# Kernel tuning notes

Measured on AMD Instinct MI355X. Metric: run time of the kernel, lower is better.

The kernel has to match this reference:

```python
import jax, jax.numpy as jnp
import numpy as np

LOSS_WEIGHT = 1.0  # init kwarg


def _cdist2(a, b):
    # Euclidean (p=2) pairwise distances via Gram trick: avoids [n,m,d] tensor.
    d2 = (jnp.sum(a * a, axis=1)[:, None]
          + jnp.sum(b * b, axis=1)[None, :]
          - 2.0 * (a @ b.T))
    return jnp.sqrt(jnp.maximum(d2, 0.0))


def _clamp_comb(f, g):
    # Composition of clamp maps x -> clip(x, lo, hi); g is applied after f.
    lf, hf = f
    lg, hg = g
    return jnp.clip(lf, lg, hg), jnp.clip(hf, lg, hg)


def _frechet(pred, target):
    c = _cdist2(pred, target)                      # [n, m]
    # First DP row: running max of c[0, :].
    row0 = jax.lax.associative_scan(jnp.maximum, c[0])

    def row_update(prev, c_row):
        # ca[i,j] = max(min(ca[i-1,j], ca[i,j-1], ca[i-1,j-1]), c[i,j])
        # For fixed i this is d[j] = clip(d[j-1], lo=c[i,j], hi=max(b[j], c[i,j]))
        # with b[j] = min(prev[j], prev[j-1]); clamp composition is associative,
        # so the whole row is a parallel associative scan (wavefront-free form).
        d0 = jnp.maximum(prev[0], c_row[0])        # ca[i,0]
        lo = c_row[1:]
        hi = jnp.maximum(jnp.minimum(prev[1:], prev[:-1]), lo)
        lo_all = jnp.concatenate([d0[None], lo])   # element 0 is the constant map d0
        hi_all = jnp.concatenate([d0[None], hi])
        lo_s, _ = jax.lax.associative_scan(_clamp_comb, (lo_all, hi_all))
        return lo_s, None

    last_row, _ = jax.lax.scan(row_update, row0, c[1:])
    return last_row[-1]


def setup_inputs() -> dict:
    key = jax.random.key(0)
    k1, k2 = jax.random.split(key)
    pred = jax.random.uniform(k1, (4096, 128), dtype=jnp.float32)
    target = jax.random.uniform(k2, (4096, 128), dtype=jnp.float32)
    return {"pred": pred, "target": target}


def reference(pred, target):
    return LOSS_WEIGHT * _frechet(pred, target)
```

## Files before the change

kernel.cpp:

```cpp
#include <hip/hip_runtime.h>

typedef unsigned short u16;
typedef unsigned int u32;
typedef __bf16 bf16x8 __attribute__((ext_vector_type(8)));
typedef float f32x4 __attribute__((ext_vector_type(4)));

#define N 4096
#define KD 128
#define NSTRIP 32
#define W 128
#define ROWB 256
#define CH 32
#define STB 16
#define NBLK 132
#define HUGEV 3.0e38f
#define TS 128
#define PADK 136

__device__ __forceinline__ u16 f2bf(float v) {
  u32 u = __float_as_uint(v);
  u += 0x7fffu + ((u >> 16) & 1u);
  return (u16)(u >> 16);
}
__device__ __forceinline__ float bf2f(u16 b) { return __uint_as_float(((u32)b) << 16); }
__device__ __forceinline__ float bfround(float v) { return bf2f(f2bf(v)); }

__device__ __forceinline__ float dpp_shr1(float oldv, float src) {
  return __int_as_float(__builtin_amdgcn_update_dpp(
      __float_as_int(oldv), __float_as_int(src), 0x138, 0xF, 0xF, false));
}

__device__ __forceinline__ void gload_lds16(const void* g, void* l) {
  __builtin_amdgcn_global_load_lds((const __attribute__((address_space(1))) u32*)g,
                                   (__attribute__((address_space(3))) u32*)l, 16, 0, 0);
}

__global__ __launch_bounds__(256) void norms_kernel(const float* __restrict__ pred,
                                                    const float* __restrict__ tgt,
                                                    float* __restrict__ na, float* __restrict__ nb,
                                                    float* __restrict__ edgeG) {
  const int t = blockIdx.x * 256 + threadIdx.x;
  if (t < NSTRIP * N) edgeG[t] = -1.0f;
  int gw = blockIdx.x * 4 + (threadIdx.x >> 6);
  int lane = threadIdx.x & 63;
  const float* base = (gw < N) ? (pred + (size_t)gw * KD) : (tgt + (size_t)(gw - N) * KD);
  float2 v = ((const float2*)base)[lane];
  float x = bfround(v.x), y = bfround(v.y);
  float s = x * x + y * y;
  #pragma unroll
  for (int off = 32; off > 0; off >>= 1) s += __shfl_xor(s, off);
  if (lane == 0) { if (gw < N) na[gw] = s; else nb[gw - N] = s; }
}

__global__ __launch_bounds__(256) void gemm_kernel(const float* __restrict__ A, const float* __restrict__ B,
                                                   const float* __restrict__ na, const float* __restrict__ nb,
                                                   u16* __restrict__ C2) {
  __shared__ u16 As[TS * PADK];
  __shared__ u16 Bs[TS * PADK];
  const int bi = blockIdx.y, bj = blockIdx.x;
  const int tid = threadIdx.x;
  {
    int row = tid >> 1, half = (tid & 1) * 64;
    const float* ga = A + (size_t)(bi * TS + row) * KD + half;
    const float* gb = B + (size_t)(bj * TS + row) * KD + half;
    u16* la = As + row * PADK + half;
    u16* lb = Bs + row * PADK + half;
    #pragma unroll
    for (int v = 0; v < 16; ++v) {
      float4 fa = ((const float4*)ga)[v];
      float4 fb = ((const float4*)gb)[v];
      *(ushort4*)(la + v * 4) = make_ushort4(f2bf(fa.x), f2bf(fa.y), f2bf(fa.z), f2bf(fa.w));
      *(ushort4*)(lb + v * 4) = make_ushort4(f2bf(fb.x), f2bf(fb.y), f2bf(fb.z), f2bf(fb.w));
    }
  }
  __syncthreads();
  const int wid = tid >> 6, lane = tid & 63;
  const int wr = (wid >> 1) * 64, wc = (wid & 1) * 64;
  const int l15 = lane & 15, l4 = lane >> 4;
  f32x4 acc[4][4] = {};
  #pragma unroll
  for (int ks = 0; ks < 4; ++ks) {
    bf16x8 af[4], bq[4];
    const int ko = ks * 32 + l4 * 8;
    #pragma unroll
    for (int m = 0; m < 4; ++m) af[m] = *(const bf16x8*)(As + (wr + m * 16 + l15) * PADK + ko);
    #pragma unroll
    for (int n = 0; n < 4; ++n) bq[n] = *(const bf16x8*)(Bs + (wc + n * 16 + l15) * PADK + ko);
    #pragma unroll
    for (int m = 0; m < 4; ++m)
      #pragma unroll
      for (int n = 0; n < 4; ++n)
        acc[m][n] = __builtin_amdgcn_mfma_f32_16x16x32_bf16(af[m], bq[n], acc[m][n], 0, 0, 0);
  }
  #pragma unroll
  for (int m = 0; m < 4; ++m) {
    const int r0 = bi * TS + wr + m * 16 + l4 * 4;
    #pragma unroll
    for (int n = 0; n < 4; ++n) {
      const int col = bj * TS + wc + n * 16 + l15;
      const float nbv = nb[col];
      #pragma unroll
      for (int e = 0; e < 4; ++e) {
        const int r = r0 + e;
        float d2v = fmaxf(na[r] + nbv - 2.0f * acc[m][n][e], 0.0f);
        C2[(size_t)r * N + col] = f2bf(d2v);
      }
    }
  }
}

#define STEPR2(CU0, CU1, EAv, EBv) { \
  const float La = dpp_shr1((EAv), E0); \
  const float Lb = dpp_shr1((EBv), D1); \
  const float c00 = __uint_as_float((CU0) << 16); \
  const float c01 = __uint_as_float((CU0) & 0xFFFF0000u); \
  const float c10 = __uint_as_float((CU1) << 16); \
  const float c11 = __uint_as_float((CU1) & 0xFFFF0000u); \
  const float o00 = fmaxf(c00, fminf(fminf(D0, Lbp), La)); \
  const float o01 = fmaxf(c01, fminf(fminf(D1, D0), o00)); \
  const float o10 = fmaxf(c10, fminf(fminf(o00, La), Lb)); \
  const float o11 = fmaxf(c11, fminf(fminf(o01, o00), o10)); \
  D0 = o10; D1 = o11; E0 = o01; Lbp = Lb; \
}

#define EOUTW { \
  if (e63) { eout[eix] = E0; eout[eix + 1] = D1; } \
  eix = (eix + 2) & 63; \
}

#define LDGR(EA4, EB4, CV, GG) { \
  EA4 = *(const float4*)(elds + 8 * (GG)); \
  EB4 = *(const float4*)(elds + 8 * (GG) + 4); \
  { const u32 a0 = cbs, a1 = (cbs + 512) & 0xFFFFu, a2 = (cbs + 1024) & 0xFFFFu, a3 = (cbs + 1536) & 0xFFFFu; \
    CV##u0 = *(const u32*)(clb + a0); CV##v0 = *(const u32*)(clb + a0 + 256); \
    CV##u1 = *(const u32*)(clb + a1); CV##v1 = *(const u32*)(clb + a1 + 256); \
    CV##u2 = *(const u32*)(clb + a2); CV##v2 = *(const u32*)(clb + a2 + 256); \
    CV##u3 = *(const u32*)(clb + a3); CV##v3 = *(const u32*)(clb + a3 + 256); } \
  cbs = (cbs + 2048) & 0xFFFFu; \
}

#define CGR(EA4, EB4, CV) { \
  STEPR2(CV##u0, CV##v0, EA4.x, EA4.y) EOUTW \
  STEPR2(CV##u1, CV##v1, EA4.z, EA4.w) EOUTW \
  STEPR2(CV##u2, CV##v2, EB4.x, EB4.y) EOUTW \
  STEPR2(CV##u3, CV##v3, EB4.z, EB4.w) EOUTW \
}

__global__ __launch_bounds__(64) void dp_kernel(const u16* __restrict__ C2, float* __restrict__ edgeG,
                                                float* __restrict__ out) {
  __shared__ u16 win[256 * W];
  __shared__ __align__(16) float elds[32];
  __shared__ __align__(16) float eout[64];
  const int bid = blockIdx.x;
  const int S = ((bid & 7) << 2) | (bid >> 3);
  const int lane = threadIdx.x;
  const u16* cbase = C2 + (size_t)S * W;
  const char* clb = (const char*)win;
  const bool s0 = (S == 0);
  const bool do_edge = (S != NSTRIP - 1);
  const bool e63 = do_edge && (lane == 63);
  const bool l32 = lane < 32;
  float* eB = edgeG + (size_t)S * N;
  float* eI = edgeG + (size_t)(S - 1) * N;

  if (s0 && l32) elds[lane] = HUGEV;

  float D0 = HUGEV, D1 = HUGEV, E0 = HUGEV;
  float Lbp = (s0 && lane == 0) ? -HUGEV : HUGEV;

  auto STAGE = [&](int c) {
    const int lrow = lane >> 4, lcol = (lane & 15) * 8;
    const u16* g0 = cbase + (size_t)(c * CH + lrow) * N + lcol;
    u16* l0 = win + ((c & 7) * CH) * W;
    #pragma unroll
    for (int n = 0; n < 8; ++n) gload_lds16(g0 + (size_t)(4 * n) * N, l0 + n * 512);
  };

  float v0p = HUGEV;
  if (S > 0 && l32)
    v0p = __hip_atomic_fetch_add(eI + lane, 0.0f, __ATOMIC_RELAXED, __HIP_MEMORY_SCOPE_AGENT);
  STAGE(0);

  for (int q = 0; q < NBLK; ++q) {
    asm volatile("s_waitcnt vmcnt(0)" ::: "memory");
    __builtin_amdgcn_sched_barrier(0);

    if (S > 0 && q <= 127) {
      int it = 0;
      while (__any(v0p < 0.0f)) {
        __builtin_amdgcn_s_sleep(1);
        if (l32)
          v0p = __hip_atomic_fetch_add(eI + q * 32 + lane, 0.0f,
                                       __ATOMIC_RELAXED, __HIP_MEMORY_SCOPE_AGENT);
        if (++it > (1 << 20)) break;
      }
      if (l32) elds[lane] = v0p;
    }

    if (S > 0 && q + 1 <= 127 && l32)
      v0p = __hip_atomic_fetch_add(eI + (q + 1) * 32 + lane, 0.0f,
                                   __ATOMIC_RELAXED, __HIP_MEMORY_SCOPE_AGENT);
    else
      v0p = HUGEV;
    if (q + 1 < 128) STAGE(q + 1);

    asm volatile("s_waitcnt lgkmcnt(0)" ::: "memory");
    __builtin_amdgcn_sched_barrier(0);

    u32 cbs = (((u32)(32 * q - 2 * lane)) & 255u) * ROWB + lane * 4;
    int eix = (32 * q - 126) & 63;

    if (q >= 4 && q <= 127) {
      float4 Aea, Aeb, Bea, Beb;
      u32 Au0, Av0, Au1, Av1, Au2, Av2, Au3, Av3;
      u32 Bu0, Bv0, Bu1, Bv1, Bu2, Bv2, Bu3, Bv3;
      LDGR(Aea, Aeb, A, 0)
      LDGR(Bea, Beb, B, 1)
      CGR(Aea, Aeb, A)
      LDGR(Aea, Aeb, A, 2)
      CGR(Bea, Beb, B)
      LDGR(Bea, Beb, B, 3)
      CGR(Aea, Aeb, A)
      CGR(Bea, Beb, B)
    } else {
      for (int k = 0; k < STB; ++k) {
        const int s = STB * q + k;
        const int i0 = 2 * (s - lane);
        const bool act = (u32)i0 <= 4094u;
        const u32 cu0 = *(const u32*)(clb + cbs);
        const u32 cu1 = *(const u32*)(clb + cbs + 256);
        cbs = (cbs + 512) & 0xFFFFu;
        const float ea = elds[(2 * k) & 31];
        const float eb = elds[(2 * k + 1) & 31];
        const float La = dpp_shr1(ea, E0);
        const float Lb = dpp_shr1(eb, D1);
        const float c00 = __uint_as_float(cu0 << 16);
        const float c01 = __uint_as_float(cu0 & 0xFFFF0000u);
        const float c10 = __uint_as_float(cu1 << 16);
        const float c11 = __uint_as_float(cu1 & 0xFFFF0000u);
        const float o00 = fmaxf(c00, fminf(fminf(D0, Lbp), La));
        const float o01 = fmaxf(c01, fminf(fminf(D1, D0), o00));
        const float o10 = fmaxf(c10, fminf(fminf(o00, La), Lb));
        const float o11 = fmaxf(c11, fminf(fminf(o01, o00), o10));
        if (act) { D0 = o10; D1 = o11; E0 = o01; Lbp = Lb; }
        if (e63 && act) { eout[i0 & 63] = o01; eout[(i0 + 1) & 63] = o11; }
      }
    }

    if (do_edge) {
      asm volatile("s_waitcnt lgkmcnt(0)" ::: "memory");
      __builtin_amdgcn_sched_barrier(0);
      const int r = 32 * q - 126 + lane;
      if (l32 && r >= 0 && r < N) {
        const float v = eout[r & 63];
        __hip_atomic_store(eB + r, v, __ATOMIC_RELAXED, __HIP_MEMORY_SCOPE_AGENT);
      }
    }
  }

  if (S == NSTRIP - 1 && lane == 63) out[0] = sqrtf(fmaxf(D1, 0.0f));
}

extern "C" void kernel_launch(void* const* d_in, const int* in_sizes, int n_in,
                              void* d_out, int out_size, void* d_ws, size_t ws_size,
                              hipStream_t stream) {
  const float* pred = (const float*)d_in[0];
  const float* tgt  = (const float*)d_in[1];
  char* ws = (char*)d_ws;
  u16* C2   = (u16*)ws;
  float* na = (float*)(ws + (size_t)N * N * 2);
  float* nb = na + N;
  float* edgeG = nb + N;
  float* out = (float*)d_out;

  hipLaunchKernelGGL(norms_kernel, dim3(2048), dim3(256), 0, stream, pred, tgt, na, nb, edgeG);
  hipLaunchKernelGGL(gemm_kernel, dim3(32, 32), dim3(256), 0, stream, pred, tgt, na, nb, C2);
  hipLaunchKernelGGL(dp_kernel, dim3(NSTRIP), dim3(64), 0, stream, C2, edgeG, out);
}
```

Measured before the change: 597.4 us.

## Split DP into 64 single-column-per-lane strips with direct edge stores

```diff
diff --git a/kernel.cpp b/kernel.cpp
--- a/kernel.cpp
+++ b/kernel.cpp
@@ -7,12 +7,13 @@
 
 #define N 4096
 #define KD 128
-#define NSTRIP 32
-#define W 128
-#define ROWB 256
+#define NSTRIP 64
+#define W 64
+#define ROWB 128
 #define CH 32
-#define STB 16
-#define NBLK 132
+#define NBLK 130
+#define RINGROWS 256
+#define WINB 32768
 #define HUGEV 3.0e38f
 #define TS 128
 #define PADK 136
@@ -109,50 +110,47 @@
   }
 }
 
-#define STEPR2(CU0, CU1, EAv, EBv) { \
-  const float La = dpp_shr1((EAv), E0); \
-  const float Lb = dpp_shr1((EBv), D1); \
-  const float c00 = __uint_as_float((CU0) << 16); \
-  const float c01 = __uint_as_float((CU0) & 0xFFFF0000u); \
-  const float c10 = __uint_as_float((CU1) << 16); \
-  const float c11 = __uint_as_float((CU1) & 0xFFFF0000u); \
-  const float o00 = fmaxf(c00, fminf(fminf(D0, Lbp), La)); \
-  const float o01 = fmaxf(c01, fminf(fminf(D1, D0), o00)); \
-  const float o10 = fmaxf(c10, fminf(fminf(o00, La), Lb)); \
-  const float o11 = fmaxf(c11, fminf(fminf(o01, o00), o10)); \
-  D0 = o10; D1 = o11; E0 = o01; Lbp = Lb; \
-}
-
-#define EOUTW { \
-  if (e63) { eout[eix] = E0; eout[eix + 1] = D1; } \
-  eix = (eix + 2) & 63; \
-}
-
-#define LDGR(EA4, EB4, CV, GG) { \
+#define EST(p, v) __hip_atomic_store((p), (v), __ATOMIC_RELAXED, __HIP_MEMORY_SCOPE_AGENT)
+
+#define STEP1(CU, EV, STI) { \
+  const float Lc = dpp_shr1((EV), D); \
+  const float c = bf2f(CU); \
+  D = fmaxf(c, fminf(fminf(D, Lp), Lc)); \
+  Lp = Lc; \
+  if (e63) EST(esb + (STI), D); \
+}
+
+#define LDG1(EA4, EB4, CV, GG) { \
   EA4 = *(const float4*)(elds + 8 * (GG)); \
   EB4 = *(const float4*)(elds + 8 * (GG) + 4); \
-  { const u32 a0 = cbs, a1 = (cbs + 512) & 0xFFFFu, a2 = (cbs + 1024) & 0xFFFFu, a3 = (cbs + 1536) & 0xFFFFu; \
-    CV##u0 = *(const u32*)(clb + a0); CV##v0 = *(const u32*)(clb + a0 + 256); \
-    CV##u1 = *(const u32*)(clb + a1); CV##v1 = *(const u32*)(clb + a1 + 256); \
-    CV##u2 = *(const u32*)(clb + a2); CV##v2 = *(const u32*)(clb + a2 + 256); \
-    CV##u3 = *(const u32*)(clb + a3); CV##v3 = *(const u32*)(clb + a3 + 256); } \
-  cbs = (cbs + 2048) & 0xFFFFu; \
-}
-
-#define CGR(EA4, EB4, CV) { \
-  STEPR2(CV##u0, CV##v0, EA4.x, EA4.y) EOUTW \
-  STEPR2(CV##u1, CV##v1, EA4.z, EA4.w) EOUTW \
-  STEPR2(CV##u2, CV##v2, EB4.x, EB4.y) EOUTW \
-  STEPR2(CV##u3, CV##v3, EB4.z, EB4.w) EOUTW \
+  CV##0 = *(const u16*)(clb + cbs); \
+  CV##1 = *(const u16*)(clb + cbs + 128); \
+  CV##2 = *(const u16*)(clb + cbs + 256); \
+  CV##3 = *(const u16*)(clb + cbs + 384); \
+  CV##4 = *(const u16*)(clb + cbs + 512); \
+  CV##5 = *(const u16*)(clb + cbs + 640); \
+  CV##6 = *(const u16*)(clb + cbs + 768); \
+  CV##7 = *(const u16*)(clb + cbs + 896); \
+  cbs = (cbs + 1024) & 0x7FFFu; \
+}
+
+#define CG1(EA4, EB4, CV, SB) { \
+  STEP1(CV##0, EA4.x, (SB) + 0) \
+  STEP1(CV##1, EA4.y, (SB) + 1) \
+  STEP1(CV##2, EA4.z, (SB) + 2) \
+  STEP1(CV##3, EA4.w, (SB) + 3) \
+  STEP1(CV##4, EB4.x, (SB) + 4) \
+  STEP1(CV##5, EB4.y, (SB) + 5) \
+  STEP1(CV##6, EB4.z, (SB) + 6) \
+  STEP1(CV##7, EB4.w, (SB) + 7) \
 }
 
 __global__ __launch_bounds__(64) void dp_kernel(const u16* __restrict__ C2, float* __restrict__ edgeG,
                                                 float* __restrict__ out) {
-  __shared__ u16 win[256 * W];
+  __shared__ u16 win[RINGROWS * W];
   __shared__ __align__(16) float elds[32];
-  __shared__ __align__(16) float eout[64];
   const int bid = blockIdx.x;
-  const int S = ((bid & 7) << 2) | (bid >> 3);
+  const int S = ((bid & 7) << 3) | (bid >> 3);
   const int lane = threadIdx.x;
   const u16* cbase = C2 + (size_t)S * W;
   const char* clb = (const char*)win;
@@ -163,17 +161,16 @@
   float* eB = edgeG + (size_t)S * N;
   float* eI = edgeG + (size_t)(S - 1) * N;
 
-  if (s0 && l32) elds[lane] = HUGEV;
-
-  float D0 = HUGEV, D1 = HUGEV, E0 = HUGEV;
-  float Lbp = (s0 && lane == 0) ? -HUGEV : HUGEV;
+  if (s0 && l32) elds[lane] = (lane == 0) ? -HUGEV : HUGEV;
+
+  float D = HUGEV, Lp = HUGEV;
 
   auto STAGE = [&](int c) {
-    const int lrow = lane >> 4, lcol = (lane & 15) * 8;
+    const int lrow = lane >> 3, lcol = (lane & 7) * 8;
     const u16* g0 = cbase + (size_t)(c * CH + lrow) * N + lcol;
     u16* l0 = win + ((c & 7) * CH) * W;
     #pragma unroll
-    for (int n = 0; n < 8; ++n) gload_lds16(g0 + (size_t)(4 * n) * N, l0 + n * 512);
+    for (int n = 0; n < 4; ++n) gload_lds16(g0 + (size_t)(8 * n) * N, l0 + n * 512);
   };
 
   float v0p = HUGEV;
@@ -182,6 +179,8 @@
   STAGE(0);
 
   for (int q = 0; q < NBLK; ++q) {
+    const int s_lo = q * CH;
+
     asm volatile("s_waitcnt vmcnt(0)" ::: "memory");
     __builtin_amdgcn_sched_barrier(0);
 
@@ -196,6 +195,7 @@
       }
       if (l32) elds[lane] = v0p;
     }
+    if (s0 && q == 1 && lane == 0) elds[0] = HUGEV;
 
     if (S > 0 && q + 1 <= 127 && l32)
       v0p = __hip_atomic_fetch_add(eI + (q + 1) * 32 + lane, 0.0f,
@@ -207,58 +207,40 @@
     asm volatile("s_waitcnt lgkmcnt(0)" ::: "memory");
     __builtin_amdgcn_sched_barrier(0);
 
-    u32 cbs = (((u32)(32 * q - 2 * lane)) & 255u) * ROWB + lane * 4;
-    int eix = (32 * q - 126) & 63;
-
-    if (q >= 4 && q <= 127) {
+    u32 cbs = (((u32)(s_lo - lane)) & 255u) * ROWB + lane * 2;
+    float* esb = eB + (s_lo - 63);
+
+    if (q >= 2 && q <= 127) {
       float4 Aea, Aeb, Bea, Beb;
-      u32 Au0, Av0, Au1, Av1, Au2, Av2, Au3, Av3;
-      u32 Bu0, Bv0, Bu1, Bv1, Bu2, Bv2, Bu3, Bv3;
-      LDGR(Aea, Aeb, A, 0)
-      LDGR(Bea, Beb, B, 1)
-      CGR(Aea, Aeb, A)
-      LDGR(Aea, Aeb, A, 2)
-      CGR(Bea, Beb, B)
-      LDGR(Bea, Beb, B, 3)
-      CGR(Aea, Aeb, A)
-      CGR(Bea, Beb, B)
+      u16 cA0, cA1, cA2, cA3, cA4, cA5, cA6, cA7;
+      u16 cB0, cB1, cB2, cB3, cB4, cB5, cB6, cB7;
+      LDG1(Aea, Aeb, cA, 0)
+      LDG1(Bea, Beb, cB, 1)
+      CG1(Aea, Aeb, cA, 0)
+      LDG1(Aea, Aeb, cA, 2)
+      CG1(Bea, Beb, cB, 8)
+      LDG1(Bea, Beb, cB, 3)
+      CG1(Aea, Aeb, cA, 16)
+      CG1(Bea, Beb, cB, 24)
     } else {
-      for (int k = 0; k < STB; ++k) {
-        const int s = STB * q + k;
-        const int i0 = 2 * (s - lane);
-        const bool act = (u32)i0 <= 4094u;
-        const u32 cu0 = *(const u32*)(clb + cbs);
-        const u32 cu1 = *(const u32*)(clb + cbs + 256);
-        cbs = (cbs + 512) & 0xFFFFu;
-        const float ea = elds[(2 * k) & 31];
-        const float eb = elds[(2 * k + 1) & 31];
-        const float La = dpp_shr1(ea, E0);
-        const float Lb = dpp_shr1(eb, D1);
-        const float c00 = __uint_as_float(cu0 << 16);
-        const float c01 = __uint_as_float(cu0 & 0xFFFF0000u);
-        const float c10 = __uint_as_float(cu1 << 16);
-        const float c11 = __uint_as_float(cu1 & 0xFFFF0000u);
-        const float o00 = fmaxf(c00, fminf(fminf(D0, Lbp), La));
-        const float o01 = fmaxf(c01, fminf(fminf(D1, D0), o00));
-        const float o10 = fmaxf(c10, fminf(fminf(o00, La), Lb));
-        const float o11 = fmaxf(c11, fminf(fminf(o01, o00), o10));
-        if (act) { D0 = o10; D1 = o11; E0 = o01; Lbp = Lb; }
-        if (e63 && act) { eout[i0 & 63] = o01; eout[(i0 + 1) & 63] = o11; }
+      for (int k = 0; k < CH; ++k) {
+        const int s = s_lo + k;
+        const u16 cu = *(const u16*)(clb + cbs);
+        cbs = (cbs + ROWB) & 0x7FFFu;
+        const float ev = elds[k & 31];
+        const float Lc = dpp_shr1(ev, D);
+        const float c = bf2f(cu);
+        const float nD = fmaxf(c, fminf(fminf(D, Lp), Lc));
+        const int i = s - lane;
+        const bool act = (u32)i < (u32)N;
+        Lp = (s0 && lane == 0) ? HUGEV : Lc;
+        if (act) D = nD;
+        if (e63 && act) EST(eB + i, nD);
       }
     }
-
-    if (do_edge) {
-      asm volatile("s_waitcnt lgkmcnt(0)" ::: "memory");
-      __builtin_amdgcn_sched_barrier(0);
-      const int r = 32 * q - 126 + lane;
-      if (l32 && r >= 0 && r < N) {
-        const float v = eout[r & 63];
-        __hip_atomic_store(eB + r, v, __ATOMIC_RELAXED, __HIP_MEMORY_SCOPE_AGENT);
-      }
-    }
-  }
-
-  if (S == NSTRIP - 1 && lane == 63) out[0] = sqrtf(fmaxf(D1, 0.0f));
+  }
+
+  if (S == NSTRIP - 1 && lane == 63) out[0] = sqrtf(fmaxf(D, 0.0f));
 }
 
 extern "C" void kernel_launch(void* const* d_in, const int* in_sizes, int n_in,
```

After: 668.0 us. 11.8% more time.
